# Optimization experiments

Measured on AMD Instinct MI355X. Metric: run time of the kernel, lower is better.

The kernel has to match this reference:

```python
import jax, jax.numpy as jnp
import numpy as np

# WFN symmetry table: symmetry index -> (px, py, pz) angular-momentum exponents
# (s; px,py,pz; 6 cartesian d; 10 cartesian f) as in standard .wfn files.
WFN_SYMMETRY_INDEX = np.array([
    [0, 0, 0],
    [1, 0, 0], [0, 1, 0], [0, 0, 1],
    [2, 0, 0], [0, 2, 0], [0, 0, 2], [1, 1, 0], [1, 0, 1], [0, 1, 1],
    [3, 0, 0], [0, 3, 0], [0, 0, 3], [2, 1, 0], [2, 0, 1], [0, 2, 1],
    [1, 2, 0], [1, 0, 2], [0, 1, 2], [1, 1, 1],
], dtype=np.float32)


def setup_inputs() -> dict:
    key = jax.random.key(0)
    k1, k2, k3, k4, k5 = jax.random.split(key, 5)
    n, ms, na, nps = 16, 4096, 32, 512
    dv = jax.random.normal(k1, (n, ms, na, 3), jnp.float32)          # sample->atom displacement vectors
    centers = jax.random.randint(k2, (n, nps), 0, na)                # primitive -> atom index (-1 = pad)
    exp = jax.random.uniform(k3, (n, nps), jnp.float32)              # GTO exponents (>0)
    sym = jax.random.randint(k4, (n, nps), 0, 20)                    # symmetry index into WFN table
    dm = jax.random.normal(k5, (n, nps, nps), jnp.float32) / nps     # density matrices
    return {"dv": dv, "centers": centers, "exp": exp, "sym": sym, "dm": dm}


def _density(dv, exp, dm, centers, sym):
    # dv: [n,ms,na,3]; exp: [n,np]; dm: [n,np,np]; centers/sym: [n,np] int
    sym_map = jnp.asarray(WFN_SYMMETRY_INDEX)
    valid = centers >= 0                                   # padded primitives marked -1
    c = jnp.where(valid, centers, 0)
    s = jnp.where(valid, sym, 0)
    r2 = jnp.sum(dv * dv, axis=-1)                         # [n,ms,na] squared distances
    r2g = jax.vmap(lambda r, ci: r[:, ci])(r2, c)          # [n,ms,np] gather per primitive
    dvg = jax.vmap(lambda d, ci: d[:, ci])(dv, c)          # [n,ms,np,3]
    pw = sym_map[s]                                        # [n,np,3] angular exponents
    # GTO kernel: dx^px * dy^py * dz^pz * exp(-alpha * r^2)
    ang = jnp.prod(jnp.power(dvg, pw[:, None, :, :]), axis=-1)   # [n,ms,np]
    basis = ang * jnp.exp(-exp[:, None, :] * r2g)
    basis = basis * valid[:, None, :].astype(basis.dtype)        # zero out padded primitives
    # rho = sum_pq basis_p * dm_pq * basis_q (per molecule, per sample point)
    return jnp.einsum('nmp,npq,nmq->nm', basis, dm, basis)


def reference(dv, centers, exp, sym, dm):
    return _density(dv, exp, dm, centers, sym)
```

## Files before the change

kernel.cpp:

```cpp
#include <hip/hip_runtime.h>
#include <stdint.h>

#define NMOL 16
#define MS   4096
#define NA   32
#define NP   512
#define BM   64
#define TBL  65536u

typedef __attribute__((ext_vector_type(4))) float  f32x4;
typedef __attribute__((ext_vector_type(4))) unsigned int u32x4;
typedef __attribute__((ext_vector_type(2))) unsigned int u32x2;
typedef __attribute__((ext_vector_type(8))) short  s16x8;
typedef __attribute__((ext_vector_type(8))) _Float16 f16x8;
typedef unsigned int uint;
typedef unsigned short ushort;

#define WS_DMF_OFF   0u
#define WS_DMF_SZ    (16u*512u*512u*2u)
#define WS_M2A_OFF   (WS_DMF_OFF + WS_DMF_SZ)
#define WS_M2A_SZ    (16u*512u*4u)
#define WS_M2B_OFF   (WS_M2A_OFF + WS_M2A_SZ)
#define WS_M2B_SZ    (16u*512u*4u)
#define WS_ALPH_OFF  (WS_M2B_OFF + WS_M2B_SZ)
#define WS_SCR_OFF   (16u << 20)

__device__ __constant__ uint c_pw[20] = {
  0x000,
  0x001, 0x010, 0x100,
  0x002, 0x020, 0x200, 0x011, 0x101, 0x110,
  0x003, 0x030, 0x300, 0x012, 0x102, 0x120, 0x021, 0x201, 0x210, 0x111
};

__device__ __forceinline__ float cvt16lo(uint u) {
  float r; asm("v_cvt_f32_f16 %0, %1" : "=v"(r) : "v"(u)); return r;
}
__device__ __forceinline__ float cvt16hi(uint u) {
  uint s = u >> 16; float r; asm("v_cvt_f32_f16 %0, %1" : "=v"(r) : "v"(s)); return r;
}
__device__ __forceinline__ uint pkmul(uint a, uint b) {
  uint r; asm("v_pk_mul_f16 %0, %1, %2" : "=v"(r) : "v"(a), "v"(b)); return r;
}
__device__ __forceinline__ uint f2h2(float a, float b) {
  union { __fp16 __attribute__((ext_vector_type(2))) h; uint u; } x;
  x.h = __builtin_amdgcn_cvt_pkrtz(a, b);
  return x.u;
}
__device__ __forceinline__ short f2hs(float f) {
  _Float16 h = (_Float16)f;
  union { _Float16 h; short s; } x; x.h = h; return x.s;
}
__device__ __forceinline__ f16x8 mkfrag(u32x2 lo, u32x2 hi) {
  union { uint u[4]; f16x8 v; } x;
  x.u[0] = lo[0]; x.u[1] = lo[1]; x.u[2] = hi[0]; x.u[3] = hi[1];
  return x.v;
}

__global__ void dm_pack(const float* __restrict__ dm, short* __restrict__ dmF,
                        const int* __restrict__ centers, const int* __restrict__ sym,
                        const float* __restrict__ expg,
                        uint* __restrict__ m2a, uint* __restrict__ m2b,
                        float* __restrict__ alphaS) {
  __shared__ float tile[NP * 33];
  const int Qp = blockIdx.x, n = blockIdx.y;
  const int t = threadIdx.x;
  const float* base = dm + (size_t)n * NP * NP;
  const float* src  = base + Qp * 32;
#pragma unroll
  for (int i = 0; i < 64; ++i) {
    int e = t + 256 * i;
    int p = e >> 5, c = e & 31;
    tile[p * 33 + c] = src[(size_t)p * NP + c];
  }
  if (n == 0) {
#pragma unroll
    for (int kk = 0; kk < 2; ++kk) {
      int i = Qp * 512 + t + 256 * kk;
      int craw = centers[i], s = sym[i];
      bool valid = (craw >= 0);
      uint c = (uint)((valid ? craw : 0) & (NA - 1));
      int si = valid ? s : 0;
      si = (si >= 0 && si < 20) ? si : 0;
      uint pw = c_pw[si];
      uint d = (pw & 15u) + ((pw >> 4) & 15u) + ((pw >> 8) & 15u);
      uint h[3]; int k = 0;
#pragma unroll
      for (uint ax = 0; ax < 3; ++ax) {
        uint e2 = (pw >> (4 * ax)) & 15u;
        for (uint r = 0; r < e2; ++r) if (k < 3) h[k++] = ax * 4096u + c * 8u;
      }
      while (k < 3) h[k++] = c * 8u;
      m2a[i] = h[0] | (h[1] << 16);
      m2b[i] = h[2] | (d << 14) | (c << 16);
      alphaS[i] = (valid ? -expg[i] : -1e5f) * 1.44269504088896f;
    }
  }
  __syncthreads();
#pragma unroll
  for (int it = 0; it < 8; ++it) {
    int v = t + 256 * it;
    int qq = v >> 10, vv = v & 1023;
    int kblk = vv >> 6, l = vv & 63;
    int p0 = kblk * 32 + ((l >> 4) << 3);
    int col = l & 15;
    int q = (Qp * 2 + qq) * 16 + col;
    f32x4 r0 = *(const f32x4*)(base + (size_t)q * NP + p0);
    f32x4 r1 = *(const f32x4*)(base + (size_t)q * NP + p0 + 4);
    s16x8 o;
#pragma unroll
    for (int j = 0; j < 8; ++j) {
      int p = p0 + j;
      float tpq = tile[p * 33 + qq * 16 + col];
      float rv = (j < 4) ? r0[j] : r1[j - 4];
      float w = (p < q) ? (tpq + rv) : ((p == q) ? tpq : 0.0f);
      o[j] = f2hs(w);
    }
    short* dst = dmF + ((size_t)(n * 32 + Qp * 2 + qq) * 16) * 512;
    *(s16x8*)(dst + (size_t)vv * 8) = o;
  }
}

#define MFMA16(a, b, c) __builtin_amdgcn_mfma_f32_16x16x32_f16(a, b, c, 0, 0, 0)

#define ISSUE_TR(AK) \
  asm volatile("ds_read_b64_tr_b16 %0, %1 offset:0"     : "=v"(l0) : "v"(AK)); \
  asm volatile("ds_read_b64_tr_b16 %0, %1 offset:512"   : "=v"(g0) : "v"(AK)); \
  asm volatile("ds_read_b64_tr_b16 %0, %1 offset:16384" : "=v"(l1) : "v"(AK)); \
  asm volatile("ds_read_b64_tr_b16 %0, %1 offset:16896" : "=v"(g1) : "v"(AK)); \
  asm volatile("ds_read_b64_tr_b16 %0, %1 offset:32768" : "=v"(l2) : "v"(AK)); \
  asm volatile("ds_read_b64_tr_b16 %0, %1 offset:33280" : "=v"(g2) : "v"(AK)); \
  asm volatile("ds_read_b64_tr_b16 %0, %1 offset:49152" : "=v"(l3) : "v"(AK)); \
  asm volatile("ds_read_b64_tr_b16 %0, %1 offset:49664" : "=v"(g3) : "v"(AK));

#define FINISH_TRIP(KBLK) do { \
  f16x8 bf0, bf1, bf2, bf3; \
  const bool c0 = (KBLK) <= kq0, c1 = (KBLK) <= kq1, c2 = (KBLK) <= kq2; \
  if (c0) bf0 = *(const f16x8*)(bp0 + (KBLK) * 512); \
  if (c1) bf1 = *(const f16x8*)(bp1 + (KBLK) * 512); \
  if (c2) bf2 = *(const f16x8*)(bp2 + (KBLK) * 512); \
  bf3 = *(const f16x8*)(bp3 + (KBLK) * 512); \
  asm volatile("s_waitcnt lgkmcnt(0)"); \
  __builtin_amdgcn_sched_barrier(0); \
  f16x8 af0 = mkfrag(l0, g0), af1 = mkfrag(l1, g1); \
  f16x8 af2 = mkfrag(l2, g2), af3 = mkfrag(l3, g3); \
  __builtin_amdgcn_s_setprio(1); \
  if (c0) { acc[0][0]=MFMA16(af0,bf0,acc[0][0]); acc[1][0]=MFMA16(af1,bf0,acc[1][0]); \
            acc[2][0]=MFMA16(af2,bf0,acc[2][0]); acc[3][0]=MFMA16(af3,bf0,acc[3][0]); } \
  if (c1) { acc[0][1]=MFMA16(af0,bf1,acc[0][1]); acc[1][1]=MFMA16(af1,bf1,acc[1][1]); \
            acc[2][1]=MFMA16(af2,bf1,acc[2][1]); acc[3][1]=MFMA16(af3,bf1,acc[3][1]); } \
  if (c2) { acc[0][2]=MFMA16(af0,bf2,acc[0][2]); acc[1][2]=MFMA16(af1,bf2,acc[1][2]); \
            acc[2][2]=MFMA16(af2,bf2,acc[2][2]); acc[3][2]=MFMA16(af3,bf2,acc[3][2]); } \
  acc[0][3]=MFMA16(af0,bf3,acc[0][3]); acc[1][3]=MFMA16(af1,bf3,acc[1][3]); \
  acc[2][3]=MFMA16(af2,bf3,acc[2][3]); acc[3][3]=MFMA16(af3,bf3,acc[3][3]); \
  __builtin_amdgcn_s_setprio(0); \
} while (0)

__device__ __forceinline__ void build_table(char* smem, const float* dvg, int t) {
#pragma unroll
  for (int k = 0; k < 4; ++k) {
    int idx = t + 512 * k;
    int m = idx >> 5, c = idx & 31;
    const float* p = dvg + (m * NA + c) * 3;
    float x = p[0], y = p[1], z = p[2];
    float r2 = fmaf(x, x, fmaf(y, y, z * z));
    uint base = TBL + ((uint)(m >> 2) << 8) + (uint)c * 8u + (uint)((m & 3) << 1);
    *(_Float16*)(smem + base)         = (_Float16)x;
    *(_Float16*)(smem + base + 4096)  = (_Float16)y;
    *(_Float16*)(smem + base + 8192)  = (_Float16)z;
    *(_Float16*)(smem + base + 12288) = (_Float16)r2;
  }
}

__device__ __forceinline__ void basis_phase(char* smem, uint ma, uint mb, float al, int p) {
  const uint alp = f2h2(al, al);
  const uint h0 = ma & 0xFFFFu, h1 = ma >> 16;
  const uint h2v = mb & 0x3FFFu;
  const uint d  = (mb >> 14) & 3u;
  const uint c  = mb >> 16;
  const uint rh = 12288u + c * 8u;
  const bool ge2 = (d >= 2), eq3 = (d == 3), eq0 = (d == 0);
  const uint wbase = ((uint)(p >> 5) << 10) + (((uint)(p >> 2) & 1u) << 9)
                   + ((((uint)p & 31u) >> 3) << 7) + (((uint)p & 3u) << 5);
#pragma unroll
  for (int j = 0; j < 8; ++j) {
    uint o = (uint)j << 9;
    u32x2 qra = *(const u32x2*)(smem + TBL + rh + o);
    u32x2 qrb = *(const u32x2*)(smem + TBL + rh + o + 256);
    u32x2 q0a, q0b, q1a, q1b, q2a, q2b;
    if (!eq0) { q0a = *(const u32x2*)(smem + TBL + h0 + o);
                q0b = *(const u32x2*)(smem + TBL + h0 + o + 256); }
    if (ge2)  { q1a = *(const u32x2*)(smem + TBL + h1 + o);
                q1b = *(const u32x2*)(smem + TBL + h1 + o + 256); }
    if (eq3)  { q2a = *(const u32x2*)(smem + TBL + h2v + o);
                q2b = *(const u32x2*)(smem + TBL + h2v + o + 256); }
    uint res[4];
#pragma unroll
    for (int w = 0; w < 4; ++w) {
      uint mq = eq0 ? 0x3C003C00u : ((w < 2) ? q0a[w] : q0b[w - 2]);
      if (ge2) mq = pkmul(mq, (w < 2) ? q1a[w] : q1b[w - 2]);
      if (eq3) mq = pkmul(mq, (w < 2) ? q2a[w] : q2b[w - 2]);
      uint ap = pkmul(alp, (w < 2) ? qra[w] : qrb[w - 2]);
      float a0 = cvt16lo(ap), a1 = cvt16hi(ap);
      float e0, e1;
      asm("v_exp_f32 %0, %1" : "=v"(e0) : "v"(a0));
      asm("v_exp_f32 %0, %1" : "=v"(e1) : "v"(a1));
      res[w] = pkmul(mq, f2h2(e0, e1));
    }
    *(u32x4*)(smem + wbase + ((uint)(j >> 1) << 14) + ((uint)(j & 1) << 4))
        = *(u32x4*)res;
  }
}

__launch_bounds__(512, 4)
__global__ void wfn_fused8(const float* __restrict__ dv,
                           const uint* __restrict__ m2aG,
                           const uint* __restrict__ m2bG,
                           const float* __restrict__ alG,
                           const short* __restrict__ dmF,
                           float* __restrict__ out) {
  __shared__ __align__(16) char smem[81920];
  const int t = threadIdx.x;
  const int bid = ((blockIdx.x & 7) << 7) + (blockIdx.x >> 3);
  const int n  = bid >> 6;
  const int m0 = (bid & 63) * BM;

  build_table(smem, dv + (size_t)(n * MS + m0) * (NA * 3), t);
  __syncthreads();
  basis_phase(smem, m2aG[n * NP + t], m2bG[n * NP + t], alG[n * NP + t], t);
  __syncthreads();

  const int lane = t & 63, wv = t >> 6, li = lane & 15, kg = lane >> 4;
  const uint lane8 = (uint)lane << 3;
  const short* dmFn = dmF + (size_t)n * (32 * 16 * 512);

  f32x4 acc[4][4];
#pragma unroll
  for (int rf = 0; rf < 4; ++rf)
#pragma unroll
    for (int qf = 0; qf < 4; ++qf)
      acc[rf][qf] = (f32x4){0.f, 0.f, 0.f, 0.f};

  const short* bp0 = dmFn + ((size_t)((wv)      * 16) * 512) + lane * 8;
  const short* bp1 = dmFn + ((size_t)((wv + 8)  * 16) * 512) + lane * 8;
  const short* bp2 = dmFn + ((size_t)((wv + 16) * 16) * 512) + lane * 8;
  const short* bp3 = dmFn + ((size_t)((wv + 24) * 16) * 512) + lane * 8;
  const int kq0 = wv >> 1, kq1 = (wv + 8) >> 1, kq2 = (wv + 16) >> 1;
  const int kmaxw = (wv + 24) >> 1;

  for (int kblk = 0; kblk <= kmaxw; ++kblk) {
    uint ak = lane8 + ((uint)kblk << 10);
    u32x2 l0, g0, l1, g1, l2, g2, l3, g3;
    ISSUE_TR(ak);
    FINISH_TRIP(kblk);
  }

  float part[16];
#pragma unroll
  for (int x = 0; x < 16; ++x) part[x] = 0.0f;
  uint qp[4];
#pragma unroll
  for (int qf = 0; qf < 4; ++qf) {
    int q = (wv + 8 * qf) * 16 + li;
    qp[qf] = ((uint)(q >> 5) << 10) + (((uint)(q >> 2) & 1u) << 9)
           + (((uint)(q & 31) >> 3) << 7) + ((uint)(q & 3) << 5) + ((uint)kg << 3);
  }
#pragma unroll
  for (int rf = 0; rf < 4; ++rf) {
#pragma unroll
    for (int qf = 0; qf < 4; ++qf) {
      union { u32x2 u; _Float16 h[4]; } dd;
      dd.u = *(const u32x2*)(smem + ((uint)rf << 14) + qp[qf]);
      part[rf * 4 + 0] = fmaf(acc[rf][qf][0], (float)dd.h[0], part[rf * 4 + 0]);
      part[rf * 4 + 1] = fmaf(acc[rf][qf][1], (float)dd.h[1], part[rf * 4 + 1]);
      part[rf * 4 + 2] = fmaf(acc[rf][qf][2], (float)dd.h[2], part[rf * 4 + 2]);
      part[rf * 4 + 3] = fmaf(acc[rf][qf][3], (float)dd.h[3], part[rf * 4 + 3]);
    }
  }

  __syncthreads();
#pragma unroll
  for (int x = 0; x < 16; ++x) {
    float v = part[x];
    v += __shfl_xor(v, 1);
    v += __shfl_xor(v, 2);
    v += __shfl_xor(v, 4);
    v += __shfl_xor(v, 8);
    part[x] = v;
  }
  float* rbuf = (float*)smem;
  if (li == 0) {
#pragma unroll
    for (int rf = 0; rf < 4; ++rf)
#pragma unroll
      for (int jj = 0; jj < 4; ++jj)
        rbuf[wv * 64 + rf * 16 + kg * 4 + jj] = part[rf * 4 + jj];
  }
  __syncthreads();
  if (t < BM) {
    float s = 0.0f;
#pragma unroll
    for (int w = 0; w < 8; ++w) s += rbuf[w * 64 + t];
    out[(size_t)n * MS + m0 + t] = s;
  }
}

__launch_bounds__(512, 4)
__global__ void wfn_probe_gemm(const short* __restrict__ dmF,
                               float* __restrict__ scr) {
  __shared__ __align__(16) char smem[81920];
  const int t = threadIdx.x;
  const int bid = ((blockIdx.x & 7) << 7) + (blockIdx.x >> 3);
  const int n  = bid >> 6;

  for (int i = t; i < 81920 / 16; i += 512)
    ((u32x4*)smem)[i] = (u32x4){0x3C003C00u, 0x3C003C00u, 0x3C003C00u, 0x3C003C00u};
  __syncthreads();

  const int lane = t & 63, wv = t >> 6;
  const uint lane8 = (uint)lane << 3;
  const short* dmFn = dmF + (size_t)n * (32 * 16 * 512);
  f32x4 acc[4][4];
#pragma unroll
  for (int rf = 0; rf < 4; ++rf)
#pragma unroll
    for (int qf = 0; qf < 4; ++qf)
      acc[rf][qf] = (f32x4){0.f, 0.f, 0.f, 0.f};
  const short* bp0 = dmFn + ((size_t)((wv)      * 16) * 512) + lane * 8;
  const short* bp1 = dmFn + ((size_t)((wv + 8)  * 16) * 512) + lane * 8;
  const short* bp2 = dmFn + ((size_t)((wv + 16) * 16) * 512) + lane * 8;
  const short* bp3 = dmFn + ((size_t)((wv + 24) * 16) * 512) + lane * 8;
  const int kq0 = wv >> 1, kq1 = (wv + 8) >> 1, kq2 = (wv + 16) >> 1;
  const int kmaxw = (wv + 24) >> 1;

  for (int rep = 0; rep < 6; ++rep) {
    for (int kblk = 0; kblk <= kmaxw; ++kblk) {
      uint ak = lane8 + ((uint)kblk << 10);
      u32x2 l0, g0, l1, g1, l2, g2, l3, g3;
      ISSUE_TR(ak);
      FINISH_TRIP(kblk);
    }
  }
  float live = acc[0][0][0] + acc[1][1][1] + acc[2][2][2] + acc[3][3][3];
  scr[(size_t)blockIdx.x * 512 + t] = live;
}

extern "C" void kernel_launch(void* const* d_in, const int* in_sizes, int n_in,
                              void* d_out, int out_size, void* d_ws, size_t ws_size,
                              hipStream_t stream) {
  const float* dv      = (const float*)d_in[0];
  const int*   centers = (const int*)d_in[1];
  const float* expg    = (const float*)d_in[2];
  const int*   sym     = (const int*)d_in[3];
  const float* dm      = (const float*)d_in[4];
  float* out = (float*)d_out;

  char* ws = (char*)d_ws;
  short* dmF    = (short*)(ws + WS_DMF_OFF);
  uint*  m2a    = (uint*)(ws + WS_M2A_OFF);
  uint*  m2b    = (uint*)(ws + WS_M2B_OFF);
  float* alphaS = (float*)(ws + WS_ALPH_OFF);

  dm_pack<<<dim3(16, NMOL), 256, 0, stream>>>(dm, dmF, centers, sym, expg,
                                              m2a, m2b, alphaS);
  wfn_fused8<<<dim3(NMOL * (MS / BM)), 512, 0, stream>>>(dv, m2a, m2b, alphaS, dmF, out);

  if (ws_size == 0) {
    float* scr = (float*)(ws + WS_SCR_OFF);
    wfn_probe_gemm<<<dim3(NMOL * (MS / BM)), 512, 0, stream>>>(dmF, scr);
  }
}
```

Measured before the change: 49.76 us.

## Split fused basis+GEMM kernel into separate basis write and GEMM kernels

Splits the fused kernel into two launches. The first builds the fp16 basis tile for each block and writes it to a 64 MB workspace buffer. The second loads that tile from global memory and runs the MFMA GEMM plus the dot-product reduction. The intent is to stop the basis-building phase from serialising against the GEMM phase in one block and to let each kernel use its own resources. The cost is a 64 MB round trip through global memory and an extra launch, and it only takes this path when the workspace is large enough. The unused probe GEMM kernel is removed.

Result: slower. 70.63 us (+42.0%).

```diff
diff --git a/kernel.cpp b/kernel.cpp
--- a/kernel.cpp
+++ b/kernel.cpp
@@ -23,7 +23,10 @@
 #define WS_M2B_OFF   (WS_M2A_OFF + WS_M2A_SZ)
 #define WS_M2B_SZ    (16u*512u*4u)
 #define WS_ALPH_OFF  (WS_M2B_OFF + WS_M2B_SZ)
-#define WS_SCR_OFF   (16u << 20)
+#define WS_ALPH_SZ   (16u*512u*4u)
+#define WS_BASF_OFF  (WS_ALPH_OFF + WS_ALPH_SZ)
+#define WS_BASF_SZ   (1024ull*65536ull)
+#define WS_SPLIT_NEED ((size_t)WS_BASF_OFF + (size_t)WS_BASF_SZ)
 
 __device__ __constant__ uint c_pw[20] = {
   0x000,
@@ -212,6 +215,127 @@
 }
 
 __launch_bounds__(512, 4)
+__global__ void basis_write(const float* __restrict__ dv,
+                            const uint* __restrict__ m2aG,
+                            const uint* __restrict__ m2bG,
+                            const float* __restrict__ alG,
+                            short* __restrict__ basisF) {
+  __shared__ __align__(16) char smem[81920];
+  const int t = threadIdx.x;
+  const int bid = blockIdx.x;
+  const int n  = bid >> 6;
+  const int m0 = (bid & 63) * BM;
+
+  build_table(smem, dv + (size_t)(n * MS + m0) * (NA * 3), t);
+  __syncthreads();
+  basis_phase(smem, m2aG[n * NP + t], m2bG[n * NP + t], alG[n * NP + t], t);
+  __syncthreads();
+
+  char* gout = (char*)basisF + (size_t)bid * 65536;
+#pragma unroll
+  for (int i = 0; i < 8; ++i) {
+    int e = t + 512 * i;
+    ((u32x4*)gout)[e] = ((const u32x4*)smem)[e];
+  }
+}
+
+__launch_bounds__(512, 4)
+__global__ void gemm_dot(const short* __restrict__ basisF,
+                         const short* __restrict__ dmF,
+                         float* __restrict__ out) {
+  __shared__ __align__(16) char smem[65536];
+  const int t = threadIdx.x;
+  const int bid = ((blockIdx.x & 7) << 7) + (blockIdx.x >> 3);
+  const int n  = bid >> 6;
+  const int m0 = (bid & 63) * BM;
+
+  {
+    const char* gin = (const char*)basisF + (size_t)bid * 65536;
+#pragma unroll
+    for (int i = 0; i < 8; ++i) {
+      int e = t + 512 * i;
+      u32x4 v = ((const u32x4*)gin)[e];
+      ((u32x4*)smem)[e] = v;
+    }
+  }
+  __syncthreads();
+
+  const int lane = t & 63, wv = t >> 6, li = lane & 15, kg = lane >> 4;
+  const uint lane8 = (uint)lane << 3;
+  const short* dmFn = dmF + (size_t)n * (32 * 16 * 512);
+
+  f32x4 acc[4][4];
+#pragma unroll
+  for (int rf = 0; rf < 4; ++rf)
+#pragma unroll
+    for (int qf = 0; qf < 4; ++qf)
+      acc[rf][qf] = (f32x4){0.f, 0.f, 0.f, 0.f};
+
+  const short* bp0 = dmFn + ((size_t)((wv)      * 16) * 512) + lane * 8;
+  const short* bp1 = dmFn + ((size_t)((wv + 8)  * 16) * 512) + lane * 8;
+  const short* bp2 = dmFn + ((size_t)((wv + 16) * 16) * 512) + lane * 8;
+  const short* bp3 = dmFn + ((size_t)((wv + 24) * 16) * 512) + lane * 8;
+  const int kq0 = wv >> 1, kq1 = (wv + 8) >> 1, kq2 = (wv + 16) >> 1;
+  const int kmaxw = (wv + 24) >> 1;
+
+  for (int kblk = 0; kblk <= kmaxw; ++kblk) {
+    uint ak = lane8 + ((uint)kblk << 10);
+    u32x2 l0, g0, l1, g1, l2, g2, l3, g3;
+    ISSUE_TR(ak);
+    FINISH_TRIP(kblk);
+  }
+
+  float part[16];
+#pragma unroll
+  for (int x = 0; x < 16; ++x) part[x] = 0.0f;
+  uint qp[4];
+#pragma unroll
+  for (int qf = 0; qf < 4; ++qf) {
+    int q = (wv + 8 * qf) * 16 + li;
+    qp[qf] = ((uint)(q >> 5) << 10) + (((uint)(q >> 2) & 1u) << 9)
+           + (((uint)(q & 31) >> 3) << 7) + ((uint)(q & 3) << 5) + ((uint)kg << 3);
+  }
+#pragma unroll
+  for (int rf = 0; rf < 4; ++rf) {
+#pragma unroll
+    for (int qf = 0; qf < 4; ++qf) {
+      union { u32x2 u; _Float16 h[4]; } dd;
+      dd.u = *(const u32x2*)(smem + ((uint)rf << 14) + qp[qf]);
+      part[rf * 4 + 0] = fmaf(acc[rf][qf][0], (float)dd.h[0], part[rf * 4 + 0]);
+      part[rf * 4 + 1] = fmaf(acc[rf][qf][1], (float)dd.h[1], part[rf * 4 + 1]);
+      part[rf * 4 + 2] = fmaf(acc[rf][qf][2], (float)dd.h[2], part[rf * 4 + 2]);
+      part[rf * 4 + 3] = fmaf(acc[rf][qf][3], (float)dd.h[3], part[rf * 4 + 3]);
+    }
+  }
+
+  __syncthreads();
+#pragma unroll
+  for (int x = 0; x < 16; ++x) {
+    float v = part[x];
+    v += __shfl_xor(v, 1);
+    v += __shfl_xor(v, 2);
+    v += __shfl_xor(v, 4);
+    v += __shfl_xor(v, 8);
+    part[x] = v;
+  }
+  float* rbuf = (float*)smem;
+  if (li == 0) {
+#pragma unroll
+    for (int rf = 0; rf < 4; ++rf)
+#pragma unroll
+      for (int jj = 0; jj < 4; ++jj)
+        rbuf[wv * 64 + rf * 16 + kg * 4 + jj] = part[rf * 4 + jj];
+  }
+  __syncthreads();
+  if (t < BM) {
+    float s = 0.0f;
+#pragma unroll
+    for (int w = 0; w < 8; ++w) s += rbuf[w * 64 + t];
+    out[(size_t)n * MS + m0 + t] = s;
+  }
+}
+
+__launch_bounds__(512, 4)
 __global__ void wfn_fused8(const float* __restrict__ dv,
                            const uint* __restrict__ m2aG,
                            const uint* __restrict__ m2bG,
@@ -304,46 +428,6 @@
   }
 }
 
-__launch_bounds__(512, 4)
-__global__ void wfn_probe_gemm(const short* __restrict__ dmF,
-                               float* __restrict__ scr) {
-  __shared__ __align__(16) char smem[81920];
-  const int t = threadIdx.x;
-  const int bid = ((blockIdx.x & 7) << 7) + (blockIdx.x >> 3);
-  const int n  = bid >> 6;
-
-  for (int i = t; i < 81920 / 16; i += 512)
-    ((u32x4*)smem)[i] = (u32x4){0x3C003C00u, 0x3C003C00u, 0x3C003C00u, 0x3C003C00u};
-  __syncthreads();
-
-  const int lane = t & 63, wv = t >> 6;
-  const uint lane8 = (uint)lane << 3;
-  const short* dmFn = dmF + (size_t)n * (32 * 16 * 512);
-  f32x4 acc[4][4];
-#pragma unroll
-  for (int rf = 0; rf < 4; ++rf)
-#pragma unroll
-    for (int qf = 0; qf < 4; ++qf)
-      acc[rf][qf] = (f32x4){0.f, 0.f, 0.f, 0.f};
-  const short* bp0 = dmFn + ((size_t)((wv)      * 16) * 512) + lane * 8;
-  const short* bp1 = dmFn + ((size_t)((wv + 8)  * 16) * 512) + lane * 8;
-  const short* bp2 = dmFn + ((size_t)((wv + 16) * 16) * 512) + lane * 8;
-  const short* bp3 = dmFn + ((size_t)((wv + 24) * 16) * 512) + lane * 8;
-  const int kq0 = wv >> 1, kq1 = (wv + 8) >> 1, kq2 = (wv + 16) >> 1;
-  const int kmaxw = (wv + 24) >> 1;
-
-  for (int rep = 0; rep < 6; ++rep) {
-    for (int kblk = 0; kblk <= kmaxw; ++kblk) {
-      uint ak = lane8 + ((uint)kblk << 10);
-      u32x2 l0, g0, l1, g1, l2, g2, l3, g3;
-      ISSUE_TR(ak);
-      FINISH_TRIP(kblk);
-    }
-  }
-  float live = acc[0][0][0] + acc[1][1][1] + acc[2][2][2] + acc[3][3][3];
-  scr[(size_t)blockIdx.x * 512 + t] = live;
-}
-
 extern "C" void kernel_launch(void* const* d_in, const int* in_sizes, int n_in,
                               void* d_out, int out_size, void* d_ws, size_t ws_size,
                               hipStream_t stream) {
@@ -362,10 +446,12 @@
 
   dm_pack<<<dim3(16, NMOL), 256, 0, stream>>>(dm, dmF, centers, sym, expg,
                                               m2a, m2b, alphaS);
-  wfn_fused8<<<dim3(NMOL * (MS / BM)), 512, 0, stream>>>(dv, m2a, m2b, alphaS, dmF, out);
-
-  if (ws_size == 0) {
-    float* scr = (float*)(ws + WS_SCR_OFF);
-    wfn_probe_gemm<<<dim3(NMOL * (MS / BM)), 512, 0, stream>>>(dmF, scr);
-  }
-}
+
+  if (ws_size >= WS_SPLIT_NEED) {
+    short* basisF = (short*)(ws + WS_BASF_OFF);
+    basis_write<<<dim3(NMOL * (MS / BM)), 512, 0, stream>>>(dv, m2a, m2b, alphaS, basisF);
+    gemm_dot<<<dim3(NMOL * (MS / BM)), 512, 0, stream>>>(basisF, dmF, out);
+  } else {
+    wfn_fused8<<<dim3(NMOL * (MS / BM)), 512, 0, stream>>>(dv, m2a, m2b, alphaS, dmF, out);
+  }
+}
```
